# Optimization experiments

Measured on AMD Instinct MI355X. Metric: run time of the kernel, lower is better.

The kernel has to match this reference:

```python
import jax, jax.numpy as jnp
import numpy as np

B, T, D = 4, 2048, 2048
DV = 1024
T_IMG, N_LAT = 8, 64
H, DH = 16, 64
INNER = H * DH
EPS = 1e-5


def setup_inputs() -> dict:
    key = jax.random.key(0)
    ks = jax.random.split(key, 8)
    x = jax.random.normal(ks[0], (B, T, D), dtype=jnp.float32)
    media = jax.random.normal(ks[1], (B, T_IMG, N_LAT, DV), dtype=jnp.float32)
    # exactly T_IMG media tokens per sequence, evenly spaced
    pos = (jnp.arange(T_IMG) + 1) * (T // (T_IMG + 1))
    media_locations = jnp.zeros((B, T), dtype=bool).at[:, pos].set(True)
    gamma = jnp.ones((D,), dtype=jnp.float32)
    beta = jnp.zeros((D,), dtype=jnp.float32)
    Wq = jax.random.normal(ks[2], (D, INNER), dtype=jnp.float32) * (D ** -0.5)
    Wkv = jax.random.normal(ks[3], (DV, 2 * INNER), dtype=jnp.float32) * (DV ** -0.5)
    Wout = jax.random.normal(ks[4], (INNER, D), dtype=jnp.float32) * (INNER ** -0.5)
    return {"x": x, "media": media, "media_locations": media_locations,
            "gamma": gamma, "beta": beta, "Wq": Wq, "Wkv": Wkv, "Wout": Wout}


def reference(x, media, media_locations, gamma, beta, Wq, Wkv, Wout):
    scale = DH ** -0.5
    # LayerNorm
    mu = jnp.mean(x, axis=-1, keepdims=True)
    var = jnp.mean(jnp.square(x - mu), axis=-1, keepdims=True)
    xn = (x - mu) * jax.lax.rsqrt(var + EPS) * gamma + beta
    q = xn @ Wq                                   # (B,T,INNER)
    media_f = media.reshape(B, T_IMG * N_LAT, DV)  # (B,J,DV)
    kv = media_f @ Wkv                             # (B,J,2*INNER)
    k, v = jnp.split(kv, 2, axis=-1)
    q = q.reshape(B, T, H, DH).transpose(0, 2, 1, 3) * scale   # (B,H,T,DH)
    k = k.reshape(B, -1, H, DH).transpose(0, 2, 1, 3)          # (B,H,J,DH)
    v = v.reshape(B, -1, H, DH).transpose(0, 2, 1, 3)
    sim = jnp.einsum('bhid,bhjd->bhij', q, k)      # (B,H,T,J)
    # media-location mask: text attends only to its immediately preceding media
    text_time = jnp.cumsum(media_locations.astype(jnp.int32), axis=-1)  # (B,T)
    media_time = jnp.arange(T_IMG, dtype=jnp.int32) + 1                 # (J_img,)
    media_time = jnp.repeat(media_time, N_LAT)                          # (J,)
    mask = text_time[:, None, :, None] == media_time[None, None, None, :]  # (B,1,T,J)
    neg = -jnp.finfo(sim.dtype).max
    sim = jnp.where(mask, sim, neg)
    sim = sim - jax.lax.stop_gradient(jnp.max(sim, axis=-1, keepdims=True))
    attn = jax.nn.softmax(sim, axis=-1)
    # zero attention for text positions with no preceding media
    no_media = (text_time == 0)[:, None, :, None]  # (B,1,T,1)
    attn = jnp.where(no_media, 0.0, attn)
    out = jnp.einsum('bhij,bhjd->bhid', attn, v)   # (B,H,T,DH)
    out = out.transpose(0, 2, 1, 3).reshape(B, T, INNER)
    return out @ Wout
```

## Files before the change

### kernel.cpp

```cpp
#include <hip/hip_runtime.h>
#include <hip/hip_bf16.h>

#define B_ 4
#define T_ 2048
#define D_ 2048
#define DV_ 1024
#define TIMG_ 8
#define NLAT_ 64
#define H_ 16
#define DH_ 64
#define INNER_ 1024
#define J_ (TIMG_ * NLAT_)

using f32x4 = __attribute__((ext_vector_type(4))) float;
using bf16x8 = __attribute__((ext_vector_type(8))) short;
using bf16x4 = __attribute__((ext_vector_type(4))) short;

__device__ __forceinline__ unsigned short f2bf(float f) {
  union { float f; unsigned int u; } c{f};
  unsigned int r = c.u + 0x7FFFu + ((c.u >> 16) & 1u);
  return (unsigned short)(r >> 16);
}

__device__ __forceinline__ void stage16(const unsigned short* g, unsigned short* l) {
  __builtin_amdgcn_global_load_lds(
      (const __attribute__((address_space(1))) unsigned int*)g,
      (__attribute__((address_space(3))) unsigned int*)l, 16, 0, 0);
}

__global__ __launch_bounds__(256) void scan_kernel(const void* __restrict__ locs,
                                                   int* __restrict__ img_idx) {
  __shared__ int sm[256];
  const int tid = threadIdx.x;
  const int b = blockIdx.x;
  const unsigned char* u8 = (const unsigned char*)locs;
  int cnt = 0;
  for (int i = tid; i < B_ * T_; i += 256) cnt += (u8[i] != 0) ? 1 : 0;
  sm[tid] = cnt;
  __syncthreads();
  for (int off = 128; off > 0; off >>= 1) {
    if (tid < off) sm[tid] += sm[tid + off];
    __syncthreads();
  }
  const bool u8mode = (sm[0] == B_ * TIMG_);
  __syncthreads();

  const int base = b * T_ + tid * 8;
  const int* i32 = (const int*)locs;
  int v[8];
  int ts = 0;
#pragma unroll
  for (int j = 0; j < 8; ++j) {
    v[j] = u8mode ? (u8[base + j] != 0 ? 1 : 0) : (i32[base + j] != 0 ? 1 : 0);
    ts += v[j];
  }
  sm[tid] = ts;
  __syncthreads();
  for (int off = 1; off < 256; off <<= 1) {
    int add = (tid >= off) ? sm[tid - off] : 0;
    __syncthreads();
    sm[tid] += add;
    __syncthreads();
  }
  int acc = sm[tid] - ts;
#pragma unroll
  for (int j = 0; j < 8; ++j) {
    acc += v[j];
    img_idx[base + j] = acc - 1;
  }
}

__global__ __launch_bounds__(256) void ln_kernel(const float* __restrict__ x,
                                                 const float* __restrict__ g,
                                                 const float* __restrict__ bta,
                                                 unsigned short* __restrict__ xn) {
  const int row = blockIdx.x;
  const int tid = threadIdx.x;
  const float4* xr = (const float4*)(x + (size_t)row * D_);
  float4 v0 = xr[tid];
  float4 v1 = xr[tid + 256];
  float s = v0.x + v0.y + v0.z + v0.w + v1.x + v1.y + v1.z + v1.w;
  float sq = v0.x * v0.x + v0.y * v0.y + v0.z * v0.z + v0.w * v0.w +
             v1.x * v1.x + v1.y * v1.y + v1.z * v1.z + v1.w * v1.w;
#pragma unroll
  for (int off = 32; off > 0; off >>= 1) {
    s += __shfl_xor(s, off);
    sq += __shfl_xor(sq, off);
  }
  __shared__ float ls[4], lq[4];
  const int lane = tid & 63, wave = tid >> 6;
  if (lane == 0) { ls[wave] = s; lq[wave] = sq; }
  __syncthreads();
  s = ls[0] + ls[1] + ls[2] + ls[3];
  sq = lq[0] + lq[1] + lq[2] + lq[3];
  const float mu = s * (1.0f / D_);
  const float rstd = rsqrtf(sq * (1.0f / D_) - mu * mu + 1e-5f);
  const float4* gv4 = (const float4*)g;
  const float4* bv4 = (const float4*)bta;
  ushort4* o4 = (ushort4*)(xn + (size_t)row * D_);
#pragma unroll
  for (int i = 0; i < 2; ++i) {
    const int idx = tid + i * 256;
    float4 vv = i == 0 ? v0 : v1;
    float4 gv = gv4[idx];
    float4 bv = bv4[idx];
    ushort4 o = make_ushort4(f2bf((vv.x - mu) * rstd * gv.x + bv.x),
                             f2bf((vv.y - mu) * rstd * gv.y + bv.y),
                             f2bf((vv.z - mu) * rstd * gv.z + bv.z),
                             f2bf((vv.w - mu) * rstd * gv.w + bv.w));
    o4[idx] = o;
  }
}

__global__ void tcast(const float* __restrict__ in, unsigned short* __restrict__ out,
                      int R, int C, float scale) {
  __shared__ float tile[32][33];
  const int bc = blockIdx.x * 32;
  const int br = blockIdx.y * 32;
  const int tx = threadIdx.x, ty = threadIdx.y;
#pragma unroll
  for (int i = ty; i < 32; i += 8)
    tile[i][tx] = in[(size_t)(br + i) * C + bc + tx];
  __syncthreads();
#pragma unroll
  for (int i = ty; i < 32; i += 8)
    out[(size_t)(bc + i) * R + br + tx] = f2bf(tile[tx][i] * scale);
}

__global__ void cast_bf16(const float* __restrict__ in, unsigned short* __restrict__ out,
                          int n4) {
  int i = blockIdx.x * blockDim.x + threadIdx.x;
  if (i >= n4) return;
  float4 v = ((const float4*)in)[i];
  ((ushort4*)out)[i] = make_ushort4(f2bf(v.x), f2bf(v.y), f2bf(v.z), f2bf(v.w));
}

__global__ void vtrans(const unsigned short* __restrict__ kvb, unsigned short* __restrict__ vt) {
  __shared__ unsigned short tile[32][33];
  const int jt = blockIdx.x * 32;
  const int dt = blockIdx.y * 32;
  const int b = blockIdx.z;
  const int tx = threadIdx.x, ty = threadIdx.y;
#pragma unroll
  for (int i = ty; i < 32; i += 8)
    tile[i][tx] = kvb[(size_t)(b * J_ + jt + i) * (2 * INNER_) + INNER_ + dt + tx];
  __syncthreads();
#pragma unroll
  for (int i = ty; i < 32; i += 8)
    vt[(size_t)(b * INNER_ + dt + i) * J_ + jt + tx] = tile[tx][i];
}

template <bool BF16OUT>
__global__ __launch_bounds__(512, 2) void gemm_8ph(const unsigned short* __restrict__ Ag,
                                                   const unsigned short* __restrict__ Bg,
                                                   void* __restrict__ Cv,
                                                   int M, int N, int K) {
  __shared__ __align__(16) unsigned short lds[2][24576];
  const int tid = threadIdx.x;
  const int lane = tid & 63;
  const int wave = tid >> 6;
  const int l15 = lane & 15;
  const int lg8 = (lane >> 4) << 3;
  const int wr64 = (wave >> 2) << 6;
  const int wc16 = (wave & 3) << 4;

  const int nwg = gridDim.x;
  int wg = ((int)blockIdx.x & 7) * (nwg >> 3) + ((int)blockIdx.x >> 3);
  const int gridM = M >> 7;
  const long row0 = (long)(wg % gridM) << 7;
  const long col0 = (long)(wg / gridM) << 8;

  auto stageA = [&](int buf, int kt, int r) {
    const int i = r * 512 + tid;
    const int row = i >> 3;
    const int c = (i & 7) ^ (row & 7);
    stage16(Ag + (size_t)(row0 + row) * K + kt + c * 8, &lds[buf][i * 8]);
  };
  auto stageB = [&](int buf, int kt, int r) {
    const int i = r * 512 + tid;
    const int row = i >> 3;
    const int c = (i & 7) ^ (row & 7);
    stage16(Bg + (size_t)(col0 + row) * K + kt + c * 8, &lds[buf][8192 + i * 8]);
  };

  const int NT = K >> 6;
  stageA(0, 0, 0); stageA(0, 0, 1);
  stageB(0, 0, 0); stageB(0, 0, 1); stageB(0, 0, 2); stageB(0, 0, 3);
  stageA(1, 64, 0); stageA(1, 64, 1);
  stageB(1, 64, 0); stageB(1, 64, 1); stageB(1, 64, 2); stageB(1, 64, 3);
  asm volatile("s_waitcnt vmcnt(6)" ::: "memory");
  asm volatile("s_barrier" ::: "memory");

  f32x4 acc[4][4] = {};
  int cur = 0;
  for (int t = 0; t < NT; ++t, cur ^= 1) {
    const unsigned short* Ab = &lds[cur][0];
    const unsigned short* Bb = &lds[cur][8192];
    bf16x8 af[4][2], bfr[4][2];
#pragma unroll
    for (int m = 0; m < 4; ++m)
#pragma unroll
      for (int kk = 0; kk < 2; ++kk) {
        const int row = wr64 + m * 16 + l15;
        af[m][kk] = *(const bf16x8*)(Ab + row * 64 + ((kk * 32 + lg8) ^ ((row & 7) << 3)));
      }
#pragma unroll
    for (int n = 0; n < 2; ++n)
#pragma unroll
      for (int kk = 0; kk < 2; ++kk) {
        const int brow = n * 64 + wc16 + l15;
        bfr[n][kk] = *(const bf16x8*)(Bb + brow * 64 + ((kk * 32 + lg8) ^ ((brow & 7) << 3)));
      }
    if (t >= 1 && t + 1 < NT) {
      stageB(cur ^ 1, (t + 1) << 6, 2); stageB(cur ^ 1, (t + 1) << 6, 3);
    }
    asm volatile("s_waitcnt vmcnt(6)" ::: "memory");
    asm volatile("s_barrier" ::: "memory");
    asm volatile("s_waitcnt lgkmcnt(0)" ::: "memory");
    __builtin_amdgcn_s_setprio(1);
#pragma unroll
    for (int m = 0; m < 4; ++m)
#pragma unroll
      for (int n = 0; n < 2; ++n)
#pragma unroll
        for (int kk = 0; kk < 2; ++kk)
          acc[m][n] = __builtin_amdgcn_mfma_f32_16x16x32_bf16(af[m][kk], bfr[n][kk], acc[m][n], 0, 0, 0);
    __builtin_amdgcn_s_setprio(0);
    asm volatile("s_barrier" ::: "memory");
#pragma unroll
    for (int n = 2; n < 4; ++n)
#pragma unroll
      for (int kk = 0; kk < 2; ++kk) {
        const int brow = n * 64 + wc16 + l15;
        bfr[n][kk] = *(const bf16x8*)(Bb + brow * 64 + ((kk * 32 + lg8) ^ ((brow & 7) << 3)));
      }
    if (t + 2 < NT) {
      stageA(cur, (t + 2) << 6, 0); stageA(cur, (t + 2) << 6, 1);
      stageB(cur, (t + 2) << 6, 0); stageB(cur, (t + 2) << 6, 1);
    }
    asm volatile("s_waitcnt vmcnt(6)" ::: "memory");
    asm volatile("s_barrier" ::: "memory");
    asm volatile("s_waitcnt lgkmcnt(0)" ::: "memory");
    __builtin_amdgcn_s_setprio(1);
#pragma unroll
    for (int m = 0; m < 4; ++m)
#pragma unroll
      for (int n = 2; n < 4; ++n)
#pragma unroll
        for (int kk = 0; kk < 2; ++kk)
          acc[m][n] = __builtin_amdgcn_mfma_f32_16x16x32_bf16(af[m][kk], bfr[n][kk], acc[m][n], 0, 0, 0);
    __builtin_amdgcn_s_setprio(0);
    asm volatile("s_barrier" ::: "memory");
  }

  const int cr = (lane >> 4) << 2;
#pragma unroll
  for (int m = 0; m < 4; ++m)
#pragma unroll
    for (int n = 0; n < 4; ++n)
#pragma unroll
      for (int j = 0; j < 4; ++j) {
        const size_t idx = (row0 + wr64 + m * 16 + cr + j) * (size_t)N + col0 + n * 64 + wc16 + l15;
        if constexpr (BF16OUT)
          ((unsigned short*)Cv)[idx] = f2bf(acc[m][n][j]);
        else
          ((float*)Cv)[idx] = acc[m][n][j];
      }
}

template <bool BF16OUT>
__global__ __launch_bounds__(512, 2) void gemm256(const unsigned short* __restrict__ Ag,
                                                  const unsigned short* __restrict__ Bg,
                                                  void* __restrict__ Cv,
                                                  int M, int N, int K) {
  __shared__ __align__(16) unsigned short lds[2][32768];
  const int tid = threadIdx.x;
  const int lane = tid & 63;
  const int wave = tid >> 6;
  const int l15 = lane & 15;
  const int lg8 = (lane >> 4) << 3;
  const int wm = (wave >> 2) << 7;
  const int wn = (wave & 3) << 6;

  const int nwg = gridDim.x;
  int wg = ((int)blockIdx.x & 7) * (nwg >> 3) + ((int)blockIdx.x >> 3);
  const int gridM = M >> 8;
  const long row0 = (long)(wg % gridM) << 8;
  const long col0 = (long)(wg / gridM) << 8;

  auto stA = [&](int buf, int kt, int r) {
    const int i = r * 512 + tid;
    const int row = i >> 3;
    const int c = (i & 7) ^ (row & 7);
    stage16(Ag + (size_t)(row0 + row) * K + kt + c * 8, &lds[buf][i * 8]);
  };
  auto stB = [&](int buf, int kt, int r) {
    const int i = r * 512 + tid;
    const int row = i >> 3;
    const int c = (i & 7) ^ (row & 7);
    stage16(Bg + (size_t)(col0 + row) * K + kt + c * 8, &lds[buf][16384 + i * 8]);
  };

  const int NT = K >> 6;
  stB(0, 0, 0); stB(0, 0, 1); stB(0, 0, 2); stB(0, 0, 3);
  stA(0, 0, 0); stA(0, 0, 1); stA(0, 0, 2); stA(0, 0, 3);
  stB(1, 64, 0); stB(1, 64, 1); stB(1, 64, 2); stB(1, 64, 3);
  asm volatile("s_waitcnt vmcnt(4)" ::: "memory");
  asm volatile("s_barrier" ::: "memory");

  f32x4 acc[8][4] = {};
  int cur = 0;
  for (int t = 0; t < NT; ++t, cur ^= 1) {
    const unsigned short* Ab = &lds[cur][0];
    const unsigned short* Bb = &lds[cur][16384];
    bf16x8 af[4][2], bfr[4][2];
    const int ktn = (t + 1) << 6;
    const int ktn2 = (t + 2) << 6;
#pragma unroll
    for (int m = 0; m < 4; ++m)
#pragma unroll
      for (int kk = 0; kk < 2; ++kk) {
        const int row = wm + m * 16 + l15;
        af[m][kk] = *(const bf16x8*)(Ab + row * 64 + ((kk * 32 + lg8) ^ ((row & 7) << 3)));
      }
#pragma unroll
    for (int n = 0; n < 2; ++n)
#pragma unroll
      for (int kk = 0; kk < 2; ++kk) {
        const int brow = wn + n * 16 + l15;
        bfr[n][kk] = *(const bf16x8*)(Bb + brow * 64 + ((kk * 32 + lg8) ^ ((brow & 7) << 3)));
      }
    if (t + 1 < NT) { stA(cur ^ 1, ktn, 0); stA(cur ^ 1, ktn, 1); }
    asm volatile("s_barrier" ::: "memory");
    asm volatile("s_waitcnt lgkmcnt(0)" ::: "memory");
    __builtin_amdgcn_s_setprio(1);
#pragma unroll
    for (int m = 0; m < 4; ++m)
#pragma unroll
      for (int n = 0; n < 2; ++n)
#pragma unroll
        for (int kk = 0; kk < 2; ++kk)
          acc[m][n] = __builtin_amdgcn_mfma_f32_16x16x32_bf16(af[m][kk], bfr[n][kk], acc[m][n], 0, 0, 0);
    __builtin_amdgcn_s_setprio(0);
    asm volatile("s_barrier" ::: "memory");
#pragma unroll
    for (int n = 2; n < 4; ++n)
#pragma unroll
      for (int kk = 0; kk < 2; ++kk) {
        const int brow = wn + n * 16 + l15;
        bfr[n][kk] = *(const bf16x8*)(Bb + brow * 64 + ((kk * 32 + lg8) ^ ((brow & 7) << 3)));
      }
    if (t + 1 < NT) { stA(cur ^ 1, ktn, 2); stA(cur ^ 1, ktn, 3); }
    asm volatile("s_barrier" ::: "memory");
    asm volatile("s_waitcnt lgkmcnt(0)" ::: "memory");
    __builtin_amdgcn_s_setprio(1);
#pragma unroll
    for (int m = 0; m < 4; ++m)
#pragma unroll
      for (int n = 2; n < 4; ++n)
#pragma unroll
        for (int kk = 0; kk < 2; ++kk)
          acc[m][n] = __builtin_amdgcn_mfma_f32_16x16x32_bf16(af[m][kk], bfr[n][kk], acc[m][n], 0, 0, 0);
    __builtin_amdgcn_s_setprio(0);
    asm volatile("s_barrier" ::: "memory");
#pragma unroll
    for (int m = 0; m < 4; ++m)
#pragma unroll
      for (int kk = 0; kk < 2; ++kk) {
        const int row = wm + (m + 4) * 16 + l15;
        af[m][kk] = *(const bf16x8*)(Ab + row * 64 + ((kk * 32 + lg8) ^ ((row & 7) << 3)));
      }
    if (t + 2 < NT) { stB(cur, ktn2, 0); stB(cur, ktn2, 1); }
    asm volatile("s_barrier" ::: "memory");
    asm volatile("s_waitcnt lgkmcnt(0)" ::: "memory");
    __builtin_amdgcn_s_setprio(1);
#pragma unroll
    for (int m = 0; m < 4; ++m)
#pragma unroll
      for (int n = 0; n < 2; ++n)
#pragma unroll
        for (int kk = 0; kk < 2; ++kk)
          acc[m + 4][n] = __builtin_amdgcn_mfma_f32_16x16x32_bf16(af[m][kk], bfr[n][kk], acc[m + 4][n], 0, 0, 0);
    __builtin_amdgcn_s_setprio(0);
    asm volatile("s_barrier" ::: "memory");
    if (t + 2 < NT) { stB(cur, ktn2, 2); stB(cur, ktn2, 3); }
    asm volatile("s_waitcnt vmcnt(4)" ::: "memory");
    asm volatile("s_barrier" ::: "memory");
    __builtin_amdgcn_s_setprio(1);
#pragma unroll
    for (int m = 0; m < 4; ++m)
#pragma unroll
      for (int n = 2; n < 4; ++n)
#pragma unroll
        for (int kk = 0; kk < 2; ++kk)
          acc[m + 4][n] = __builtin_amdgcn_mfma_f32_16x16x32_bf16(af[m][kk], bfr[n][kk], acc[m + 4][n], 0, 0, 0);
    __builtin_amdgcn_s_setprio(0);
    asm volatile("s_barrier" ::: "memory");
  }

  const int cr = (lane >> 4) << 2;
#pragma unroll
  for (int m = 0; m < 8; ++m)
#pragma unroll
    for (int n = 0; n < 4; ++n)
#pragma unroll
      for (int j = 0; j < 4; ++j) {
        const size_t idx = (row0 + wm + m * 16 + cr + j) * (size_t)N + col0 + wn + n * 16 + l15;
        if constexpr (BF16OUT)
          ((unsigned short*)Cv)[idx] = f2bf(acc[m][n][j]);
        else
          ((float*)Cv)[idx] = acc[m][n][j];
      }
}

__global__ __launch_bounds__(256) void attn2_kernel(
    const unsigned short* __restrict__ qb,
    const unsigned short* __restrict__ kvb,
    const unsigned short* __restrict__ vt,
    const int* __restrict__ img_idx,
    unsigned short* __restrict__ attn_out) {
  __shared__ unsigned short Pl[4][64 * 72];
  const int tid = threadIdx.x;
  const int lane = tid & 63;
  const int w = tid >> 6;
  int bid = blockIdx.x;
  const int hg = bid & 3; bid >>= 2;
  const int tile = bid & 31; bid >>= 5;
  const int b = bid;
  const int t0 = tile * 64;
  const int h = hg * 4 + w;
  const int l15 = lane & 15;
  const int lg = lane >> 4;

  const int* ii = img_idx + b * T_ + t0;
  int myimg = ii[lane];
  int tmin = myimg, tmax = myimg;
#pragma unroll
  for (int off = 1; off < 64; off <<= 1) {
    tmin = min(tmin, __shfl_xor(tmin, off));
    tmax = max(tmax, __shfl_xor(tmax, off));
  }
  unsigned short* op = attn_out + (size_t)(b * T_ + t0) * INNER_ + h * DH_;
  if (tmin < 0) {
    for (int r = 0; r < 64; ++r)
      if (ii[r] < 0) op[(size_t)r * INNER_ + lane] = 0;
  }
  if (tmax < 0) return;

  bf16x8 qa[4][2];
  const unsigned short* qrow = qb + (size_t)(b * T_ + t0) * INNER_ + h * DH_;
#pragma unroll
  for (int m = 0; m < 4; ++m)
#pragma unroll
    for (int kk = 0; kk < 2; ++kk)
      qa[m][kk] = *(const bf16x8*)(qrow + (size_t)(l15 + m * 16) * INNER_ + kk * 32 + lg * 8);

  unsigned short* pw = Pl[w];
  for (int img = max(tmin, 0); img <= tmax; ++img) {
    const unsigned short* Kb = kvb + (size_t)(b * J_ + img * NLAT_) * (2 * INNER_) + h * DH_;
    f32x4 acc[4][4] = {};
#pragma unroll
    for (int kk = 0; kk < 2; ++kk) {
      bf16x8 bfr[4];
#pragma unroll
      for (int n = 0; n < 4; ++n)
        bfr[n] = *(const bf16x8*)(Kb + (size_t)(l15 + n * 16) * (2 * INNER_) + kk * 32 + lg * 8);
#pragma unroll
      for (int m = 0; m < 4; ++m)
#pragma unroll
        for (int n = 0; n < 4; ++n)
          acc[m][n] = __builtin_amdgcn_mfma_f32_16x16x32_bf16(qa[m][kk], bfr[n], acc[m][n], 0, 0, 0);
    }
#pragma unroll
    for (int m = 0; m < 4; ++m) {
#pragma unroll
      for (int j = 0; j < 4; ++j) {
        float mx = fmaxf(fmaxf(acc[m][0][j], acc[m][1][j]), fmaxf(acc[m][2][j], acc[m][3][j]));
#pragma unroll
        for (int off = 1; off < 16; off <<= 1) mx = fmaxf(mx, __shfl_xor(mx, off));
        float sum = 0.f;
#pragma unroll
        for (int n = 0; n < 4; ++n) {
          float e = __expf(acc[m][n][j] - mx);
          acc[m][n][j] = e;
          sum += e;
        }
#pragma unroll
        for (int off = 1; off < 16; off <<= 1) sum += __shfl_xor(sum, off);
        const float ri = 1.0f / sum;
        const int row = m * 16 + lg * 4 + j;
#pragma unroll
        for (int n = 0; n < 4; ++n)
          pw[row * 72 + n * 16 + l15] = f2bf(acc[m][n][j] * ri);
      }
    }
    const unsigned short* Vb = vt + (size_t)(b * INNER_ + h * DH_) * J_ + img * NLAT_;
    f32x4 oacc[4][4] = {};
#pragma unroll
    for (int kk = 0; kk < 2; ++kk) {
      bf16x8 pa[4], bfr[4];
#pragma unroll
      for (int m = 0; m < 4; ++m) {
        bf16x4 lo = *(const bf16x4*)(pw + (m * 16 + l15) * 72 + kk * 32 + lg * 8);
        bf16x4 hi = *(const bf16x4*)(pw + (m * 16 + l15) * 72 + kk * 32 + lg * 8 + 4);
        bf16x8 v;
#pragma unroll
        for (int e = 0; e < 4; ++e) { v[e] = lo[e]; v[e + 4] = hi[e]; }
        pa[m] = v;
      }
#pragma unroll
      for (int n = 0; n < 4; ++n)
        bfr[n] = *(const bf16x8*)(Vb + (size_t)(l15 + n * 16) * J_ + kk * 32 + lg * 8);
#pragma unroll
      for (int m = 0; m < 4; ++m)
#pragma unroll
        for (int n = 0; n < 4; ++n)
          oacc[m][n] = __builtin_amdgcn_mfma_f32_16x16x32_bf16(pa[m], bfr[n], oacc[m][n], 0, 0, 0);
    }
#pragma unroll
    for (int m = 0; m < 4; ++m)
#pragma unroll
      for (int j = 0; j < 4; ++j) {
        const int row = m * 16 + lg * 4 + j;
        if (ii[row] == img) {
#pragma unroll
          for (int n = 0; n < 4; ++n)
            op[(size_t)row * INNER_ + n * 16 + l15] = f2bf(oacc[m][n][j]);
        }
      }
  }
}

extern "C" void kernel_launch(void* const* d_in, const int* in_sizes, int n_in,
                              void* d_out, int out_size, void* d_ws, size_t ws_size,
                              hipStream_t stream) {
  const float* x = (const float*)d_in[0];
  const float* media = (const float*)d_in[1];
  const void* mloc = d_in[2];
  const float* gamma = (const float*)d_in[3];
  const float* beta = (const float*)d_in[4];
  const float* Wq = (const float*)d_in[5];
  const float* Wkv = (const float*)d_in[6];
  const float* Wout = (const float*)d_in[7];
  float* out = (float*)d_out;

  char* ws = (char*)d_ws;
  unsigned short* xn = (unsigned short*)(ws);
  unsigned short* wqt = (unsigned short*)(ws + 33554432);
  unsigned short* wkvt = (unsigned short*)(ws + 37748736);
  unsigned short* woutt = (unsigned short*)(ws + 41943040);
  unsigned short* medb = (unsigned short*)(ws + 46137344);
  unsigned short* qb = (unsigned short*)(ws + 50331648);
  unsigned short* kvb = (unsigned short*)(ws + 67108864);
  unsigned short* vt = (unsigned short*)(ws + 75497472);
  int* img_idx = (int*)(ws + 79691776);
  unsigned short* attn_out = xn;

  scan_kernel<<<B_, 256, 0, stream>>>(mloc, img_idx);
  ln_kernel<<<B_ * T_, 256, 0, stream>>>(x, gamma, beta, xn);
  tcast<<<dim3(INNER_ / 32, D_ / 32), dim3(32, 8), 0, stream>>>(Wq, wqt, D_, INNER_, 0.125f);
  tcast<<<dim3(2 * INNER_ / 32, DV_ / 32), dim3(32, 8), 0, stream>>>(Wkv, wkvt, DV_, 2 * INNER_, 1.0f);
  tcast<<<dim3(D_ / 32, INNER_ / 32), dim3(32, 8), 0, stream>>>(Wout, woutt, INNER_, D_, 1.0f);
  cast_bf16<<<(B_ * J_ * DV_ / 4 + 255) / 256, 256, 0, stream>>>(media, medb, B_ * J_ * DV_ / 4);
  gemm_8ph<true><<<(B_ * T_ / 128) * (INNER_ / 256), 512, 0, stream>>>(xn, wqt, qb, B_ * T_, INNER_, D_);
  gemm_8ph<true><<<(B_ * J_ / 128) * (2 * INNER_ / 256), 512, 0, stream>>>(medb, wkvt, kvb, B_ * J_, 2 * INNER_, DV_);
  vtrans<<<dim3(J_ / 32, INNER_ / 32, B_), dim3(32, 8), 0, stream>>>(kvb, vt);
  attn2_kernel<<<B_ * (T_ / 64) * 4, 256, 0, stream>>>(qb, kvb, vt, img_idx, attn_out);
  gemm256<false><<<(B_ * T_ / 256) * (D_ / 256), 512, 0, stream>>>(attn_out, woutt, out, B_ * T_, D_, INNER_);
}
```

Before: 164.6 us.

## Merge prep kernels into one launch and triple-buffer B tiles in GEMM

Six preprocessing launches (scan, layernorm, three weight transpose-casts, media cast) become one kernel that dispatches on block index. This removes launch gaps and tail idling between the small kernels. The projection GEMM now keeps the B operand in a three-slot LDS ring (A stays double-buffered) and reorders its prefetches so the loads for t+2 are issued earlier. LDS use rises from 96KB to 128KB per block, which could lower occupancy, and the new vmcnt accounting has to stay correct.

```diff
diff --git a/kernel.cpp b/kernel.cpp
--- a/kernel.cpp
+++ b/kernel.cpp
@@ -28,111 +28,124 @@
       (__attribute__((address_space(3))) unsigned int*)l, 16, 0, 0);
 }
 
-__global__ __launch_bounds__(256) void scan_kernel(const void* __restrict__ locs,
-                                                   int* __restrict__ img_idx) {
-  __shared__ int sm[256];
+__global__ __launch_bounds__(256) void prep_kernel(
+    const float* __restrict__ x, const void* __restrict__ locs,
+    const float* __restrict__ g, const float* __restrict__ bta,
+    const float* __restrict__ Wq, const float* __restrict__ Wkv,
+    const float* __restrict__ Wout, const float* __restrict__ media,
+    unsigned short* __restrict__ xn, int* __restrict__ img_idx,
+    unsigned short* __restrict__ wqt, unsigned short* __restrict__ wkvt,
+    unsigned short* __restrict__ woutt, unsigned short* __restrict__ medb) {
+  __shared__ __align__(16) float smf[1056];
   const int tid = threadIdx.x;
-  const int b = blockIdx.x;
-  const unsigned char* u8 = (const unsigned char*)locs;
-  int cnt = 0;
-  for (int i = tid; i < B_ * T_; i += 256) cnt += (u8[i] != 0) ? 1 : 0;
-  sm[tid] = cnt;
-  __syncthreads();
-  for (int off = 128; off > 0; off >>= 1) {
-    if (tid < off) sm[tid] += sm[tid + off];
+  int blk = blockIdx.x;
+
+  if (blk < 8192) {
+    const int row = blk;
+    const float4* xr = (const float4*)(x + (size_t)row * D_);
+    float4 v0 = xr[tid];
+    float4 v1 = xr[tid + 256];
+    float s = v0.x + v0.y + v0.z + v0.w + v1.x + v1.y + v1.z + v1.w;
+    float sq = v0.x * v0.x + v0.y * v0.y + v0.z * v0.z + v0.w * v0.w +
+               v1.x * v1.x + v1.y * v1.y + v1.z * v1.z + v1.w * v1.w;
+#pragma unroll
+    for (int off = 32; off > 0; off >>= 1) {
+      s += __shfl_xor(s, off);
+      sq += __shfl_xor(sq, off);
+    }
+    const int lane = tid & 63, wave = tid >> 6;
+    if (lane == 0) { smf[wave] = s; smf[4 + wave] = sq; }
     __syncthreads();
-  }
-  const bool u8mode = (sm[0] == B_ * TIMG_);
-  __syncthreads();
-
-  const int base = b * T_ + tid * 8;
-  const int* i32 = (const int*)locs;
-  int v[8];
-  int ts = 0;
-#pragma unroll
-  for (int j = 0; j < 8; ++j) {
-    v[j] = u8mode ? (u8[base + j] != 0 ? 1 : 0) : (i32[base + j] != 0 ? 1 : 0);
-    ts += v[j];
-  }
-  sm[tid] = ts;
-  __syncthreads();
-  for (int off = 1; off < 256; off <<= 1) {
-    int add = (tid >= off) ? sm[tid - off] : 0;
-    __syncthreads();
-    sm[tid] += add;
-    __syncthreads();
-  }
-  int acc = sm[tid] - ts;
-#pragma unroll
-  for (int j = 0; j < 8; ++j) {
-    acc += v[j];
-    img_idx[base + j] = acc - 1;
-  }
-}
-
-__global__ __launch_bounds__(256) void ln_kernel(const float* __restrict__ x,
-                                                 const float* __restrict__ g,
-                                                 const float* __restrict__ bta,
-                                                 unsigned short* __restrict__ xn) {
-  const int row = blockIdx.x;
-  const int tid = threadIdx.x;
-  const float4* xr = (const float4*)(x + (size_t)row * D_);
-  float4 v0 = xr[tid];
-  float4 v1 = xr[tid + 256];
-  float s = v0.x + v0.y + v0.z + v0.w + v1.x + v1.y + v1.z + v1.w;
-  float sq = v0.x * v0.x + v0.y * v0.y + v0.z * v0.z + v0.w * v0.w +
-             v1.x * v1.x + v1.y * v1.y + v1.z * v1.z + v1.w * v1.w;
-#pragma unroll
-  for (int off = 32; off > 0; off >>= 1) {
-    s += __shfl_xor(s, off);
-    sq += __shfl_xor(sq, off);
-  }
-  __shared__ float ls[4], lq[4];
-  const int lane = tid & 63, wave = tid >> 6;
-  if (lane == 0) { ls[wave] = s; lq[wave] = sq; }
-  __syncthreads();
-  s = ls[0] + ls[1] + ls[2] + ls[3];
-  sq = lq[0] + lq[1] + lq[2] + lq[3];
-  const float mu = s * (1.0f / D_);
-  const float rstd = rsqrtf(sq * (1.0f / D_) - mu * mu + 1e-5f);
-  const float4* gv4 = (const float4*)g;
-  const float4* bv4 = (const float4*)bta;
-  ushort4* o4 = (ushort4*)(xn + (size_t)row * D_);
-#pragma unroll
-  for (int i = 0; i < 2; ++i) {
-    const int idx = tid + i * 256;
-    float4 vv = i == 0 ? v0 : v1;
-    float4 gv = gv4[idx];
-    float4 bv = bv4[idx];
-    ushort4 o = make_ushort4(f2bf((vv.x - mu) * rstd * gv.x + bv.x),
+    s = smf[0] + smf[1] + smf[2] + smf[3];
+    sq = smf[4] + smf[5] + smf[6] + smf[7];
+    const float mu = s * (1.0f / D_);
+    const float rstd = rsqrtf(sq * (1.0f / D_) - mu * mu + 1e-5f);
+    const float4* gv4 = (const float4*)g;
+    const float4* bv4 = (const float4*)bta;
+    ushort4* o4 = (ushort4*)(xn + (size_t)row * D_);
+#pragma unroll
+    for (int i = 0; i < 2; ++i) {
+      const int idx = tid + i * 256;
+      float4 vv = i == 0 ? v0 : v1;
+      float4 gv = gv4[idx];
+      float4 bv = bv4[idx];
+      o4[idx] = make_ushort4(f2bf((vv.x - mu) * rstd * gv.x + bv.x),
                              f2bf((vv.y - mu) * rstd * gv.y + bv.y),
                              f2bf((vv.z - mu) * rstd * gv.z + bv.z),
                              f2bf((vv.w - mu) * rstd * gv.w + bv.w));
-    o4[idx] = o;
-  }
-}
-
-__global__ void tcast(const float* __restrict__ in, unsigned short* __restrict__ out,
-                      int R, int C, float scale) {
-  __shared__ float tile[32][33];
-  const int bc = blockIdx.x * 32;
-  const int br = blockIdx.y * 32;
-  const int tx = threadIdx.x, ty = threadIdx.y;
+    }
+    return;
+  }
+  blk -= 8192;
+  if (blk < 4) {
+    int* sm = (int*)smf;
+    const int b = blk;
+    const unsigned char* u8 = (const unsigned char*)locs;
+    int cnt = 0;
+    for (int i = tid; i < B_ * T_; i += 256) cnt += (u8[i] != 0) ? 1 : 0;
+    sm[tid] = cnt;
+    __syncthreads();
+    for (int off = 128; off > 0; off >>= 1) {
+      if (tid < off) sm[tid] += sm[tid + off];
+      __syncthreads();
+    }
+    const bool u8mode = (sm[0] == B_ * TIMG_);
+    __syncthreads();
+    const int base = b * T_ + tid * 8;
+    const int* i32 = (const int*)locs;
+    int v[8];
+    int ts = 0;
+#pragma unroll
+    for (int j = 0; j < 8; ++j) {
+      v[j] = u8mode ? (u8[base + j] != 0 ? 1 : 0) : (i32[base + j] != 0 ? 1 : 0);
+      ts += v[j];
+    }
+    sm[tid] = ts;
+    __syncthreads();
+    for (int off = 1; off < 256; off <<= 1) {
+      int add = (tid >= off) ? sm[tid - off] : 0;
+      __syncthreads();
+      sm[tid] += add;
+      __syncthreads();
+    }
+    int acc = sm[tid] - ts;
+#pragma unroll
+    for (int j = 0; j < 8; ++j) {
+      acc += v[j];
+      img_idx[base + j] = acc - 1;
+    }
+    return;
+  }
+  blk -= 4;
+  const int tx = tid & 31, ty = tid >> 5;
+  float (*tile)[33] = (float(*)[33])smf;
+  const float* tin = nullptr;
+  unsigned short* tout = nullptr;
+  int R = 0, C = 0, bx = 0, by = 0;
+  float scale = 1.0f;
+  if (blk < 2048) {
+    tin = Wq; tout = wqt; R = D_; C = INNER_; bx = blk & 31; by = blk >> 5; scale = 0.125f;
+  } else if (blk < 4096) {
+    blk -= 2048;
+    tin = Wkv; tout = wkvt; R = DV_; C = 2 * INNER_; bx = blk & 63; by = blk >> 6;
+  } else if (blk < 6144) {
+    blk -= 4096;
+    tin = Wout; tout = woutt; R = INNER_; C = D_; bx = blk & 63; by = blk >> 6;
+  } else {
+    blk -= 6144;
+    const int i = blk * 256 + tid;
+    float4 v = ((const float4*)media)[i];
+    ((ushort4*)medb)[i] = make_ushort4(f2bf(v.x), f2bf(v.y), f2bf(v.z), f2bf(v.w));
+    return;
+  }
+  const int bc = bx * 32, br = by * 32;
 #pragma unroll
   for (int i = ty; i < 32; i += 8)
-    tile[i][tx] = in[(size_t)(br + i) * C + bc + tx];
+    tile[i][tx] = tin[(size_t)(br + i) * C + bc + tx];
   __syncthreads();
 #pragma unroll
   for (int i = ty; i < 32; i += 8)
-    out[(size_t)(bc + i) * R + br + tx] = f2bf(tile[tx][i] * scale);
-}
-
-__global__ void cast_bf16(const float* __restrict__ in, unsigned short* __restrict__ out,
-                          int n4) {
-  int i = blockIdx.x * blockDim.x + threadIdx.x;
-  if (i >= n4) return;
-  float4 v = ((const float4*)in)[i];
-  ((ushort4*)out)[i] = make_ushort4(f2bf(v.x), f2bf(v.y), f2bf(v.z), f2bf(v.w));
+    tout[(size_t)(bc + i) * R + br + tx] = f2bf(tile[tx][i] * scale);
 }
 
 __global__ void vtrans(const unsigned short* __restrict__ kvb, unsigned short* __restrict__ vt) {
@@ -151,11 +164,11 @@
 }
 
 template <bool BF16OUT>
-__global__ __launch_bounds__(512, 2) void gemm_8ph(const unsigned short* __restrict__ Ag,
+__global__ __launch_bounds__(512, 2) void gemm_bt2(const unsigned short* __restrict__ Ag,
                                                    const unsigned short* __restrict__ Bg,
                                                    void* __restrict__ Cv,
                                                    int M, int N, int K) {
-  __shared__ __align__(16) unsigned short lds[2][24576];
+  __shared__ __align__(16) unsigned short lds[65536];
   const int tid = threadIdx.x;
   const int lane = tid & 63;
   const int wave = tid >> 6;
@@ -170,32 +183,32 @@
   const long row0 = (long)(wg % gridM) << 7;
   const long col0 = (long)(wg / gridM) << 8;
 
-  auto stageA = [&](int buf, int kt, int r) {
+  auto stA = [&](int t, int r) {
     const int i = r * 512 + tid;
     const int row = i >> 3;
     const int c = (i & 7) ^ (row & 7);
-    stage16(Ag + (size_t)(row0 + row) * K + kt + c * 8, &lds[buf][i * 8]);
+    stage16(Ag + (size_t)(row0 + row) * K + (t << 6) + c * 8,
+            &lds[(t & 1) * 8192 + i * 8]);
   };
-  auto stageB = [&](int buf, int kt, int r) {
+  auto stB = [&](int t, int r) {
     const int i = r * 512 + tid;
     const int row = i >> 3;
     const int c = (i & 7) ^ (row & 7);
-    stage16(Bg + (size_t)(col0 + row) * K + kt + c * 8, &lds[buf][8192 + i * 8]);
+    stage16(Bg + (size_t)(col0 + row) * K + (t << 6) + c * 8,
+            &lds[16384 + (t % 3) * 16384 + i * 8]);
   };
 
   const int NT = K >> 6;
-  stageA(0, 0, 0); stageA(0, 0, 1);
-  stageB(0, 0, 0); stageB(0, 0, 1); stageB(0, 0, 2); stageB(0, 0, 3);
-  stageA(1, 64, 0); stageA(1, 64, 1);
-  stageB(1, 64, 0); stageB(1, 64, 1); stageB(1, 64, 2); stageB(1, 64, 3);
-  asm volatile("s_waitcnt vmcnt(6)" ::: "memory");
+  stB(0, 0); stB(0, 1); stB(0, 2); stB(0, 3);
+  stA(0, 0); stA(0, 1);
+  stB(1, 0); stB(1, 1); stB(1, 2); stB(1, 3);
+  asm volatile("s_waitcnt vmcnt(4)" ::: "memory");
   asm volatile("s_barrier" ::: "memory");
 
   f32x4 acc[4][4] = {};
-  int cur = 0;
-  for (int t = 0; t < NT; ++t, cur ^= 1) {
-    const unsigned short* Ab = &lds[cur][0];
-    const unsigned short* Bb = &lds[cur][8192];
+  for (int t = 0; t < NT; ++t) {
+    const unsigned short* Ab = &lds[(t & 1) * 8192];
+    const unsigned short* Bb = &lds[16384 + (t % 3) * 16384];
     bf16x8 af[4][2], bfr[4][2];
 #pragma unroll
     for (int m = 0; m < 4; ++m)
@@ -211,10 +224,8 @@
         const int brow = n * 64 + wc16 + l15;
         bfr[n][kk] = *(const bf16x8*)(Bb + brow * 64 + ((kk * 32 + lg8) ^ ((brow & 7) << 3)));
       }
-    if (t >= 1 && t + 1 < NT) {
-      stageB(cur ^ 1, (t + 1) << 6, 2); stageB(cur ^ 1, (t + 1) << 6, 3);
-    }
-    asm volatile("s_waitcnt vmcnt(6)" ::: "memory");
+    if (t + 1 < NT) { stA(t + 1, 0); stA(t + 1, 1); }
+    if (t + 2 < NT) { stB(t + 2, 0); stB(t + 2, 1); }
     asm volatile("s_barrier" ::: "memory");
     asm volatile("s_waitcnt lgkmcnt(0)" ::: "memory");
     __builtin_amdgcn_s_setprio(1);
@@ -235,10 +246,11 @@
         bfr[n][kk] = *(const bf16x8*)(Bb + brow * 64 + ((kk * 32 + lg8) ^ ((brow & 7) << 3)));
       }
     if (t + 2 < NT) {
-      stageA(cur, (t + 2) << 6, 0); stageA(cur, (t + 2) << 6, 1);
-      stageB(cur, (t + 2) << 6, 0); stageB(cur, (t + 2) << 6, 1);
-    }
-    asm volatile("s_waitcnt vmcnt(6)" ::: "memory");
+      stB(t + 2, 2); stB(t + 2, 3);
+      asm volatile("s_waitcnt vmcnt(4)" ::: "memory");
+    } else {
+      asm volatile("s_waitcnt vmcnt(0)" ::: "memory");
+    }
     asm volatile("s_barrier" ::: "memory");
     asm volatile("s_waitcnt lgkmcnt(0)" ::: "memory");
     __builtin_amdgcn_s_setprio(1);
@@ -556,14 +568,10 @@
   int* img_idx = (int*)(ws + 79691776);
   unsigned short* attn_out = xn;
 
-  scan_kernel<<<B_, 256, 0, stream>>>(mloc, img_idx);
-  ln_kernel<<<B_ * T_, 256, 0, stream>>>(x, gamma, beta, xn);
-  tcast<<<dim3(INNER_ / 32, D_ / 32), dim3(32, 8), 0, stream>>>(Wq, wqt, D_, INNER_, 0.125f);
-  tcast<<<dim3(2 * INNER_ / 32, DV_ / 32), dim3(32, 8), 0, stream>>>(Wkv, wkvt, DV_, 2 * INNER_, 1.0f);
-  tcast<<<dim3(D_ / 32, INNER_ / 32), dim3(32, 8), 0, stream>>>(Wout, woutt, INNER_, D_, 1.0f);
-  cast_bf16<<<(B_ * J_ * DV_ / 4 + 255) / 256, 256, 0, stream>>>(media, medb, B_ * J_ * DV_ / 4);
-  gemm_8ph<true><<<(B_ * T_ / 128) * (INNER_ / 256), 512, 0, stream>>>(xn, wqt, qb, B_ * T_, INNER_, D_);
-  gemm_8ph<true><<<(B_ * J_ / 128) * (2 * INNER_ / 256), 512, 0, stream>>>(medb, wkvt, kvb, B_ * J_, 2 * INNER_, DV_);
+  prep_kernel<<<16388, 256, 0, stream>>>(x, mloc, gamma, beta, Wq, Wkv, Wout, media,
+                                         xn, img_idx, wqt, wkvt, woutt, medb);
+  gemm_bt2<true><<<(B_ * T_ / 128) * (INNER_ / 256), 512, 0, stream>>>(xn, wqt, qb, B_ * T_, INNER_, D_);
+  gemm_bt2<true><<<(B_ * J_ / 128) * (2 * INNER_ / 256), 512, 0, stream>>>(medb, wkvt, kvb, B_ * J_, 2 * INNER_, DV_);
   vtrans<<<dim3(J_ / 32, INNER_ / 32, B_), dim3(32, 8), 0, stream>>>(kvb, vt);
   attn2_kernel<<<B_ * (T_ / 64) * 4, 256, 0, stream>>>(qb, kvb, vt, img_idx, attn_out);
   gemm256<false><<<(B_ * T_ / 256) * (D_ / 256), 512, 0, stream>>>(attn_out, woutt, out, B_ * T_, D_, INNER_);
```

After: 153.6 us. -6.7%, faster.
